# Performance work log

Measured on AMD Instinct MI355X. Metric: run time of the kernel, lower is better.

## Reference

```python
import jax, jax.numpy as jnp
import numpy as np

B, A, V, D = 16, 1024, 1024, 512


def setup_inputs() -> dict:
    key = jax.random.key(0)
    k1, k2 = jax.random.split(key)
    audio_encoded = jax.random.normal(k1, (B, A, D), dtype=jnp.float32)
    visual_encoded = jax.random.normal(k2, (B, V, D), dtype=jnp.float32)
    return {"audio_encoded": audio_encoded, "visual_encoded": visual_encoded}


def reference(audio_encoded, visual_encoded):
    # Batched pairwise L2 distance: out[b, a, v] = ||audio[b,a] - visual[b,v]||_2
    # Fused ||a||^2 + ||v||^2 - 2 a.v formulation (single batched GEMM) replacing
    # the original per-(batch, audio-frame) Python loop of diff/pow/sum/sqrt.
    a_sq = jnp.sum(audio_encoded * audio_encoded, axis=-1)   # [B, A]
    v_sq = jnp.sum(visual_encoded * visual_encoded, axis=-1)  # [B, V]
    cross = jnp.einsum("bad,bvd->bav", audio_encoded, visual_encoded)  # [B, A, V]
    dist_sq = a_sq[:, :, None] + v_sq[:, None, :] - 2.0 * cross
    dist_sq = jnp.maximum(dist_sq, 0.0)  # clamp fp round-off negatives
    l2_features = jnp.sqrt(dist_sq)  # [B, A, V]
    return l2_features
```

## Files before the change

### kernel.cpp

```cpp
#include <hip/hip_runtime.h>
#include <hip/hip_bf16.h>

typedef __attribute__((ext_vector_type(8))) short short8;
typedef __attribute__((ext_vector_type(4))) float fv4;
typedef __attribute__((ext_vector_type(4))) int   iv4;

constexpr int B_ = 16, A_ = 1024, V_ = 1024, D_ = 512;
constexpr int ROWS_A = B_ * A_;
constexpr int ROWS_T = 2 * ROWS_A;
constexpr size_t BF_ONE = (size_t)ROWS_A * D_ * 2;
constexpr size_t WS_NEED = 2 * BF_ONE + (size_t)ROWS_T * 4;

__device__ __forceinline__ unsigned f2bf(float f) {
    unsigned u = __builtin_bit_cast(unsigned, f);
    return (u + 0x7fffu + ((u >> 16) & 1u)) >> 16;
}

__global__ void __launch_bounds__(256)
convert_kernel(const float* __restrict__ audio, const float* __restrict__ visual,
               ushort* __restrict__ abf, ushort* __restrict__ vbf,
               float* __restrict__ normA, float* __restrict__ normV)
{
    const int lane = threadIdx.x & 63;
    const int wv   = (blockIdx.x * 256 + threadIdx.x) >> 6;
    const int nw   = (gridDim.x * 256) >> 6;

    for (int row = wv; row < ROWS_T; row += nw) {
        const float* src; ushort* dst; float* nd; int r;
        if (row < ROWS_A) { src = audio;  dst = abf; nd = normA; r = row; }
        else              { src = visual; dst = vbf; nd = normV; r = row - ROWS_A; }

        const float* p = src + (size_t)r * D_ + lane * 8;
        fv4 x0 = *(const fv4*)p;
        fv4 x1 = *(const fv4*)(p + 4);

        float s = 0.f;
#pragma unroll
        for (int i = 0; i < 4; ++i) s += x0[i] * x0[i] + x1[i] * x1[i];

        iv4 w;
        w[0] = (int)(f2bf(x0[0]) | (f2bf(x0[1]) << 16));
        w[1] = (int)(f2bf(x0[2]) | (f2bf(x0[3]) << 16));
        w[2] = (int)(f2bf(x1[0]) | (f2bf(x1[1]) << 16));
        w[3] = (int)(f2bf(x1[2]) | (f2bf(x1[3]) << 16));
        *(iv4*)(dst + (size_t)r * D_ + lane * 8) = w;

#pragma unroll
        for (int m = 1; m < 64; m <<= 1) s += __shfl_xor(s, m, 64);
        if (lane == 0) nd[r] = s;
    }
}

__device__ __forceinline__ void gload16(const void* g, void* l) {
    __builtin_amdgcn_global_load_lds((const __attribute__((address_space(1))) void*)g,
                                     (__attribute__((address_space(3))) void*)l,
                                     16, 0, 0);
}
__device__ __forceinline__ unsigned lds_addr(const void* p) {
    return (unsigned)(unsigned long long)(__attribute__((address_space(3))) const char*)p;
}
__device__ __forceinline__ short8 dsr128(unsigned a) {
    short8 r;
    asm volatile("ds_read_b128 %0, %1" : "=v"(r) : "v"(a));
    return r;
}
#define SB0()   __builtin_amdgcn_sched_barrier(0)
#define LGK0()  asm volatile("s_waitcnt lgkmcnt(0)")
#define VMCN(n) asm volatile("s_waitcnt vmcnt(" #n ")")
#define RBAR()  do { SB0(); __builtin_amdgcn_s_barrier(); SB0(); } while (0)

__global__ void __launch_bounds__(256, 2)
gemm128(const ushort* __restrict__ abf, const ushort* __restrict__ vbf,
        const float* __restrict__ normA, const float* __restrict__ normV,
        float* __restrict__ out)
{
    __shared__ __align__(16) char sA[2][128 * 128];
    __shared__ __align__(16) char sB[2][128 * 128];
    __shared__ float lnrm[256];

    const int t = threadIdx.x, lane = t & 63, w = t >> 6;
    const int wm = w >> 1, wn = w & 1;

    const int orig = blockIdx.x;
    const int wg   = (orig & 7) * 128 + (orig >> 3);
    const int b = wg >> 6, tile = wg & 63, ab = tile >> 3, vb = tile & 7;

    const ushort* Ag = abf + ((size_t)b * A_ + ab * 128) * D_;
    const ushort* Vg = vbf + ((size_t)b * V_ + vb * 128) * D_;

    const int rl = lane >> 3;
    const int cs = (lane & 7) ^ rl;
    const ushort* asrc = Ag + (size_t)(w * 32 + rl) * D_ + cs * 8;
    const ushort* vsrc = Vg + (size_t)(w * 32 + rl) * D_ + cs * 8;

#define STAGE(kt, buf) do {                                           \
        const size_t _ko = (size_t)(kt) * 64;                         \
        char* _da = (char*)sA[buf] + w * 32 * 128;                    \
        char* _db = (char*)sB[buf] + w * 32 * 128;                    \
        gload16(asrc + 0 * 8 * D_ + _ko, _da + 0 * 1024);             \
        gload16(vsrc + 0 * 8 * D_ + _ko, _db + 0 * 1024);             \
        gload16(asrc + 1 * 8 * D_ + _ko, _da + 1 * 1024);             \
        gload16(vsrc + 1 * 8 * D_ + _ko, _db + 1 * 1024);             \
        gload16(asrc + 2 * 8 * D_ + _ko, _da + 2 * 1024);             \
        gload16(vsrc + 2 * 8 * D_ + _ko, _db + 2 * 1024);             \
        gload16(asrc + 3 * 8 * D_ + _ko, _da + 3 * 1024);             \
        gload16(vsrc + 3 * 8 * D_ + _ko, _db + 3 * 1024);             \
    } while (0)

    if (t < 128) lnrm[t] = normA[(size_t)b * A_ + ab * 128 + t];
    else         lnrm[t] = normV[(size_t)b * V_ + vb * 128 + (t - 128)];
    __syncthreads();

    STAGE(0, 0);
    STAGE(1, 1);
    VMCN(8);
    RBAR();

    fv4 acc[4][4];
#pragma unroll
    for (int m = 0; m < 4; ++m)
#pragma unroll
        for (int n = 0; n < 4; ++n) acc[m][n] = fv4{0.f, 0.f, 0.f, 0.f};

    const int frow = lane & 15, fg = lane >> 4, xk = frow & 7;
    const unsigned cof0 = (unsigned)(((0 + fg) ^ xk) << 4);
    const unsigned cof1 = (unsigned)(((4 + fg) ^ xk) << 4);
    const unsigned baseA = lds_addr(&sA[0][0]);
    const unsigned baseB = lds_addr(&sB[0][0]);
    const unsigned arow = (unsigned)((wm * 64 + frow) * 128);
    const unsigned brow = (unsigned)((wn * 64 + frow) * 128);

#pragma unroll 1
    for (int kt = 0; kt < 8; ++kt) {
        const int cur = kt & 1;
        const unsigned Ab = baseA + (unsigned)cur * 16384u + arow;
        const unsigned Bb = baseB + (unsigned)cur * 16384u + brow;

        short8 av[4][2];
        {
            short8 bv[2][2];
#pragma unroll
            for (int m = 0; m < 4; ++m) {
                av[m][0] = dsr128(Ab + m * 2048 + cof0);
                av[m][1] = dsr128(Ab + m * 2048 + cof1);
            }
#pragma unroll
            for (int n = 0; n < 2; ++n) {
                bv[n][0] = dsr128(Bb + n * 2048 + cof0);
                bv[n][1] = dsr128(Bb + n * 2048 + cof1);
            }
            LGK0(); SB0();
            __builtin_amdgcn_s_setprio(1);
#pragma unroll
            for (int k = 0; k < 2; ++k)
#pragma unroll
                for (int m = 0; m < 4; ++m)
#pragma unroll
                    for (int n = 0; n < 2; ++n)
                        acc[m][n] = __builtin_amdgcn_mfma_f32_16x16x32_bf16(av[m][k], bv[n][k], acc[m][n], 0, 0, 0);
            __builtin_amdgcn_s_setprio(0);
        }
        {
            short8 bv[2][2];
#pragma unroll
            for (int n = 0; n < 2; ++n) {
                bv[n][0] = dsr128(Bb + (n + 2) * 2048 + cof0);
                bv[n][1] = dsr128(Bb + (n + 2) * 2048 + cof1);
            }
            LGK0(); SB0();
            __builtin_amdgcn_s_setprio(1);
#pragma unroll
            for (int k = 0; k < 2; ++k)
#pragma unroll
                for (int m = 0; m < 4; ++m)
#pragma unroll
                    for (int n = 0; n < 2; ++n)
                        acc[m][n + 2] = __builtin_amdgcn_mfma_f32_16x16x32_bf16(av[m][k], bv[n][k], acc[m][n + 2], 0, 0, 0);
            __builtin_amdgcn_s_setprio(0);
        }

        if (kt < 7) {
            RBAR();
            if (kt < 6) {
                STAGE(kt + 2, cur);
                VMCN(8);
            } else {
                VMCN(0);
            }
            RBAR();
        }
    }

    float* Ob = out + (size_t)b * A_ * V_ + (size_t)(ab * 128) * V_ + vb * 128;
#pragma unroll
    for (int m = 0; m < 4; ++m) {
#pragma unroll
        for (int n = 0; n < 4; ++n) {
            const int col = wn * 64 + n * 16 + frow;
            const float vsq = lnrm[128 + col];
#pragma unroll
            for (int j = 0; j < 4; ++j) {
                const int row = wm * 64 + m * 16 + fg * 4 + j;
                float d2 = lnrm[row] + vsq - 2.f * acc[m][n][j];
                Ob[(size_t)row * V_ + col] = sqrtf(fmaxf(d2, 0.f));
            }
        }
    }
#undef STAGE
}

__global__ void __launch_bounds__(256)
l2dist_naive(const float* __restrict__ audio, const float* __restrict__ visual,
             float* __restrict__ out)
{
    const size_t idx = (size_t)blockIdx.x * 256 + threadIdx.x;
    const size_t total = (size_t)B_ * A_ * V_;
    if (idx >= total) return;
    const int v = idx & (V_ - 1);
    const int a = (idx >> 10) & (A_ - 1);
    const int b = idx >> 20;
    const float* ap = audio  + ((size_t)b * A_ + a) * D_;
    const float* vp = visual + ((size_t)b * V_ + v) * D_;
    float s = 0.f;
    for (int d = 0; d < D_; ++d) {
        float df = ap[d] - vp[d];
        s += df * df;
    }
    out[idx] = sqrtf(s);
}

extern "C" void kernel_launch(void* const* d_in, const int* in_sizes, int n_in,
                              void* d_out, int out_size, void* d_ws, size_t ws_size,
                              hipStream_t stream) {
    const float* audio  = (const float*)d_in[0];
    const float* visual = (const float*)d_in[1];
    float* out = (float*)d_out;

    if (ws_size >= WS_NEED) {
        char* ws = (char*)d_ws;
        ushort* abf = (ushort*)ws;
        ushort* vbf = (ushort*)(ws + BF_ONE);
        float*  nA  = (float*)(ws + 2 * BF_ONE);
        float*  nV  = nA + ROWS_A;
        convert_kernel<<<2048, 256, 0, stream>>>(audio, visual, abf, vbf, nA, nV);
        gemm128<<<1024, 256, 0, stream>>>(abf, vbf, nA, nV, out);
    } else {
        const size_t total = (size_t)B_ * A_ * V_;
        l2dist_naive<<<(int)((total + 255) / 256), 256, 0, stream>>>(audio, visual, out);
    }
}
```

Baseline: 49.54 us.

## Enlarge GEMM tile to 256x256 with 512-thread blocks and restructured pipeline

Replaces the 128x128 tile GEMM (256 threads, 2 blocks per CU) with a 256x256 tile using 8 waves, each computing 128x64. LDS doubles to hold larger double-buffered tiles, and the launch drops to 256 blocks, roughly one per CU. The k-loop now waits and synchronises at the top and issues the next stage after the compute, with B and A fragments reloaded in phases. The aim is to cut redundant global and L2 loads through more operand reuse. The cost is no overlap between blocks on a CU, so every CU hits its epilogue store burst at the same time, plus higher register and LDS pressure.

After: 49.49 us. Within noise of the previous version (-0.1%).

```diff
diff --git a/kernel.cpp b/kernel.cpp
--- a/kernel.cpp
+++ b/kernel.cpp
@@ -69,56 +69,54 @@
 #define VMCN(n) asm volatile("s_waitcnt vmcnt(" #n ")")
 #define RBAR()  do { SB0(); __builtin_amdgcn_s_barrier(); SB0(); } while (0)
 
-__global__ void __launch_bounds__(256, 2)
-gemm128(const ushort* __restrict__ abf, const ushort* __restrict__ vbf,
+__global__ void __launch_bounds__(512, 1)
+gemm256(const ushort* __restrict__ abf, const ushort* __restrict__ vbf,
         const float* __restrict__ normA, const float* __restrict__ normV,
         float* __restrict__ out)
 {
-    __shared__ __align__(16) char sA[2][128 * 128];
-    __shared__ __align__(16) char sB[2][128 * 128];
-    __shared__ float lnrm[256];
+    __shared__ __align__(16) char sA[2][256 * 128];
+    __shared__ __align__(16) char sB[2][256 * 128];
+    __shared__ float lnrm[512];
 
     const int t = threadIdx.x, lane = t & 63, w = t >> 6;
-    const int wm = w >> 1, wn = w & 1;
+    const int wm = w >> 2, wn = w & 3;
 
     const int orig = blockIdx.x;
-    const int wg   = (orig & 7) * 128 + (orig >> 3);
-    const int b = wg >> 6, tile = wg & 63, ab = tile >> 3, vb = tile & 7;
-
-    const ushort* Ag = abf + ((size_t)b * A_ + ab * 128) * D_;
-    const ushort* Vg = vbf + ((size_t)b * V_ + vb * 128) * D_;
+    const int wg   = (orig & 7) * 32 + (orig >> 3);
+    const int b = wg >> 4, tile = wg & 15, ab = tile >> 2, vb = tile & 3;
+
+    const ushort* Ag = abf + ((size_t)b * A_ + ab * 256) * D_;
+    const ushort* Vg = vbf + ((size_t)b * V_ + vb * 256) * D_;
 
     const int rl = lane >> 3;
     const int cs = (lane & 7) ^ rl;
-    const ushort* asrc = Ag + (size_t)(w * 32 + rl) * D_ + cs * 8;
-    const ushort* vsrc = Vg + (size_t)(w * 32 + rl) * D_ + cs * 8;
-
-#define STAGE(kt, buf) do {                                           \
-        const size_t _ko = (size_t)(kt) * 64;                         \
-        char* _da = (char*)sA[buf] + w * 32 * 128;                    \
-        char* _db = (char*)sB[buf] + w * 32 * 128;                    \
-        gload16(asrc + 0 * 8 * D_ + _ko, _da + 0 * 1024);             \
-        gload16(vsrc + 0 * 8 * D_ + _ko, _db + 0 * 1024);             \
-        gload16(asrc + 1 * 8 * D_ + _ko, _da + 1 * 1024);             \
-        gload16(vsrc + 1 * 8 * D_ + _ko, _db + 1 * 1024);             \
-        gload16(asrc + 2 * 8 * D_ + _ko, _da + 2 * 1024);             \
-        gload16(vsrc + 2 * 8 * D_ + _ko, _db + 2 * 1024);             \
-        gload16(asrc + 3 * 8 * D_ + _ko, _da + 3 * 1024);             \
-        gload16(vsrc + 3 * 8 * D_ + _ko, _db + 3 * 1024);             \
+    const ushort* asrc = Ag + (size_t)(w * 8 + rl) * D_ + cs * 8;
+    const ushort* vsrc = Vg + (size_t)(w * 8 + rl) * D_ + cs * 8;
+
+#define STAGE(kt, buf) do {                                               \
+        const size_t _ko = (size_t)(kt) * 64;                             \
+        char* _da = (char*)sA[buf] + w * 8 * 128;                         \
+        char* _db = (char*)sB[buf] + w * 8 * 128;                         \
+        gload16(asrc + 0 * 64 * D_ + _ko, _da + 0 * 64 * 128);            \
+        gload16(vsrc + 0 * 64 * D_ + _ko, _db + 0 * 64 * 128);            \
+        gload16(asrc + 1 * 64 * D_ + _ko, _da + 1 * 64 * 128);            \
+        gload16(vsrc + 1 * 64 * D_ + _ko, _db + 1 * 64 * 128);            \
+        gload16(asrc + 2 * 64 * D_ + _ko, _da + 2 * 64 * 128);            \
+        gload16(vsrc + 2 * 64 * D_ + _ko, _db + 2 * 64 * 128);            \
+        gload16(asrc + 3 * 64 * D_ + _ko, _da + 3 * 64 * 128);            \
+        gload16(vsrc + 3 * 64 * D_ + _ko, _db + 3 * 64 * 128);            \
     } while (0)
 
-    if (t < 128) lnrm[t] = normA[(size_t)b * A_ + ab * 128 + t];
-    else         lnrm[t] = normV[(size_t)b * V_ + vb * 128 + (t - 128)];
+    if (t < 256) lnrm[t] = normA[(size_t)b * A_ + ab * 256 + t];
+    else         lnrm[t] = normV[(size_t)b * V_ + vb * 256 + (t - 256)];
     __syncthreads();
 
     STAGE(0, 0);
     STAGE(1, 1);
-    VMCN(8);
-    RBAR();
-
-    fv4 acc[4][4];
-#pragma unroll
-    for (int m = 0; m < 4; ++m)
+
+    fv4 acc[8][4];
+#pragma unroll
+    for (int m = 0; m < 8; ++m)
 #pragma unroll
         for (int n = 0; n < 4; ++n) acc[m][n] = fv4{0.f, 0.f, 0.f, 0.f};
 
@@ -127,80 +125,97 @@
     const unsigned cof1 = (unsigned)(((4 + fg) ^ xk) << 4);
     const unsigned baseA = lds_addr(&sA[0][0]);
     const unsigned baseB = lds_addr(&sB[0][0]);
-    const unsigned arow = (unsigned)((wm * 64 + frow) * 128);
+    const unsigned arow = (unsigned)((wm * 128 + frow) * 128);
     const unsigned brow = (unsigned)((wn * 64 + frow) * 128);
+
+    short8 av[4][2], bv[4][2];
 
 #pragma unroll 1
     for (int kt = 0; kt < 8; ++kt) {
         const int cur = kt & 1;
-        const unsigned Ab = baseA + (unsigned)cur * 16384u + arow;
-        const unsigned Bb = baseB + (unsigned)cur * 16384u + brow;
-
-        short8 av[4][2];
-        {
-            short8 bv[2][2];
-#pragma unroll
-            for (int m = 0; m < 4; ++m) {
-                av[m][0] = dsr128(Ab + m * 2048 + cof0);
-                av[m][1] = dsr128(Ab + m * 2048 + cof1);
-            }
-#pragma unroll
-            for (int n = 0; n < 2; ++n) {
-                bv[n][0] = dsr128(Bb + n * 2048 + cof0);
-                bv[n][1] = dsr128(Bb + n * 2048 + cof1);
-            }
-            LGK0(); SB0();
-            __builtin_amdgcn_s_setprio(1);
-#pragma unroll
-            for (int k = 0; k < 2; ++k)
-#pragma unroll
-                for (int m = 0; m < 4; ++m)
-#pragma unroll
-                    for (int n = 0; n < 2; ++n)
-                        acc[m][n] = __builtin_amdgcn_mfma_f32_16x16x32_bf16(av[m][k], bv[n][k], acc[m][n], 0, 0, 0);
-            __builtin_amdgcn_s_setprio(0);
-        }
-        {
-            short8 bv[2][2];
-#pragma unroll
-            for (int n = 0; n < 2; ++n) {
-                bv[n][0] = dsr128(Bb + (n + 2) * 2048 + cof0);
-                bv[n][1] = dsr128(Bb + (n + 2) * 2048 + cof1);
-            }
-            LGK0(); SB0();
-            __builtin_amdgcn_s_setprio(1);
-#pragma unroll
-            for (int k = 0; k < 2; ++k)
-#pragma unroll
-                for (int m = 0; m < 4; ++m)
-#pragma unroll
-                    for (int n = 0; n < 2; ++n)
-                        acc[m][n + 2] = __builtin_amdgcn_mfma_f32_16x16x32_bf16(av[m][k], bv[n][k], acc[m][n + 2], 0, 0, 0);
-            __builtin_amdgcn_s_setprio(0);
-        }
-
-        if (kt < 7) {
-            RBAR();
-            if (kt < 6) {
-                STAGE(kt + 2, cur);
-                VMCN(8);
-            } else {
-                VMCN(0);
-            }
-            RBAR();
-        }
-    }
-
-    float* Ob = out + (size_t)b * A_ * V_ + (size_t)(ab * 128) * V_ + vb * 128;
-#pragma unroll
-    for (int m = 0; m < 4; ++m) {
+        const unsigned Ab = baseA + (unsigned)cur * 32768u + arow;
+        const unsigned Bb = baseB + (unsigned)cur * 32768u + brow;
+
+        if (kt < 7) { VMCN(8); } else { VMCN(0); }
+        RBAR();
+
+#pragma unroll
+        for (int m = 0; m < 4; ++m) {
+            av[m][0] = dsr128(Ab + m * 2048 + cof0);
+            av[m][1] = dsr128(Ab + m * 2048 + cof1);
+        }
+#pragma unroll
+        for (int n = 0; n < 2; ++n) {
+            bv[n][0] = dsr128(Bb + n * 2048 + cof0);
+            bv[n][1] = dsr128(Bb + n * 2048 + cof1);
+        }
+        LGK0(); SB0();
+        __builtin_amdgcn_s_setprio(1);
+#pragma unroll
+        for (int k = 0; k < 2; ++k)
+#pragma unroll
+            for (int m = 0; m < 4; ++m)
+#pragma unroll
+                for (int n = 0; n < 2; ++n)
+                    acc[m][n] = __builtin_amdgcn_mfma_f32_16x16x32_bf16(av[m][k], bv[n][k], acc[m][n], 0, 0, 0);
+        __builtin_amdgcn_s_setprio(0);
+
+#pragma unroll
+        for (int n = 2; n < 4; ++n) {
+            bv[n][0] = dsr128(Bb + n * 2048 + cof0);
+            bv[n][1] = dsr128(Bb + n * 2048 + cof1);
+        }
+        LGK0(); SB0();
+        __builtin_amdgcn_s_setprio(1);
+#pragma unroll
+        for (int k = 0; k < 2; ++k)
+#pragma unroll
+            for (int m = 0; m < 4; ++m)
+#pragma unroll
+                for (int n = 2; n < 4; ++n)
+                    acc[m][n] = __builtin_amdgcn_mfma_f32_16x16x32_bf16(av[m][k], bv[n][k], acc[m][n], 0, 0, 0);
+        __builtin_amdgcn_s_setprio(0);
+
+#pragma unroll
+        for (int m = 0; m < 4; ++m) {
+            av[m][0] = dsr128(Ab + (m + 4) * 2048 + cof0);
+            av[m][1] = dsr128(Ab + (m + 4) * 2048 + cof1);
+        }
+        LGK0(); SB0();
+        __builtin_amdgcn_s_setprio(1);
+#pragma unroll
+        for (int k = 0; k < 2; ++k)
+#pragma unroll
+            for (int m = 0; m < 4; ++m)
+#pragma unroll
+                for (int n = 2; n < 4; ++n)
+                    acc[m + 4][n] = __builtin_amdgcn_mfma_f32_16x16x32_bf16(av[m][k], bv[n][k], acc[m + 4][n], 0, 0, 0);
+        __builtin_amdgcn_s_setprio(0);
+
+        __builtin_amdgcn_s_setprio(1);
+#pragma unroll
+        for (int k = 0; k < 2; ++k)
+#pragma unroll
+            for (int m = 0; m < 4; ++m)
+#pragma unroll
+                for (int n = 0; n < 2; ++n)
+                    acc[m + 4][n] = __builtin_amdgcn_mfma_f32_16x16x32_bf16(av[m][k], bv[n][k], acc[m + 4][n], 0, 0, 0);
+        __builtin_amdgcn_s_setprio(0);
+
+        RBAR();
+        if (kt < 6) STAGE(kt + 2, cur);
+    }
+
+    float* Ob = out + (size_t)b * A_ * V_ + (size_t)(ab * 256) * V_ + vb * 256;
+#pragma unroll
+    for (int m = 0; m < 8; ++m) {
 #pragma unroll
         for (int n = 0; n < 4; ++n) {
             const int col = wn * 64 + n * 16 + frow;
-            const float vsq = lnrm[128 + col];
+            const float vsq = lnrm[256 + col];
 #pragma unroll
             for (int j = 0; j < 4; ++j) {
-                const int row = wm * 64 + m * 16 + fg * 4 + j;
+                const int row = wm * 128 + m * 16 + fg * 4 + j;
                 float d2 = lnrm[row] + vsq - 2.f * acc[m][n][j];
                 Ob[(size_t)row * V_ + col] = sqrtf(fmaxf(d2, 0.f));
             }
@@ -243,7 +258,7 @@
         float*  nA  = (float*)(ws + 2 * BF_ONE);
         float*  nV  = nA + ROWS_A;
         convert_kernel<<<2048, 256, 0, stream>>>(audio, visual, abf, vbf, nA, nV);
-        gemm128<<<1024, 256, 0, stream>>>(abf, vbf, nA, nV, out);
+        gemm256<<<256, 512, 0, stream>>>(abf, vbf, nA, nV, out);
     } else {
         const size_t total = (size_t)B_ * A_ * V_;
         l2dist_naive<<<(int)((total + 255) / 256), 256, 0, stream>>>(audio, visual, out);
```

## Drop LDS double buffering for single buffer and higher occupancy

Applied to the files above, without the earlier changes.

Replaces the two-stage LDS ping-pong with a single 32 KB buffer and raises the launch bound from 2 to 4 blocks per CU. Each k-step now syncs, issues the global-to-LDS loads for the next tile, and syncs again, leaving the compiler to insert the vmcnt wait. The aim is to hide memory latency through more resident workgroups instead of in-block prefetch. In exchange, loads no longer overlap with MFMA work inside a block, and the tighter register budget from the higher launch bound may cause spills.

Result: slower. 60.69 us (+22.5%).

```diff
diff --git a/kernel.cpp b/kernel.cpp
--- a/kernel.cpp
+++ b/kernel.cpp
@@ -64,18 +64,16 @@
     asm volatile("ds_read_b128 %0, %1" : "=v"(r) : "v"(a));
     return r;
 }
-#define SB0()   __builtin_amdgcn_sched_barrier(0)
-#define LGK0()  asm volatile("s_waitcnt lgkmcnt(0)")
-#define VMCN(n) asm volatile("s_waitcnt vmcnt(" #n ")")
-#define RBAR()  do { SB0(); __builtin_amdgcn_s_barrier(); SB0(); } while (0)
-
-__global__ void __launch_bounds__(256, 2)
+#define SB0()  __builtin_amdgcn_sched_barrier(0)
+#define LGK0() asm volatile("s_waitcnt lgkmcnt(0)")
+
+__global__ void __launch_bounds__(256, 4)
 gemm128(const ushort* __restrict__ abf, const ushort* __restrict__ vbf,
         const float* __restrict__ normA, const float* __restrict__ normV,
         float* __restrict__ out)
 {
-    __shared__ __align__(16) char sA[2][128 * 128];
-    __shared__ __align__(16) char sB[2][128 * 128];
+    __shared__ __align__(16) char sA[128 * 128];
+    __shared__ __align__(16) char sB[128 * 128];
     __shared__ float lnrm[256];
 
     const int t = threadIdx.x, lane = t & 63, w = t >> 6;
@@ -93,10 +91,10 @@
     const ushort* asrc = Ag + (size_t)(w * 32 + rl) * D_ + cs * 8;
     const ushort* vsrc = Vg + (size_t)(w * 32 + rl) * D_ + cs * 8;
 
-#define STAGE(kt, buf) do {                                           \
+#define STAGE(kt) do {                                                \
         const size_t _ko = (size_t)(kt) * 64;                         \
-        char* _da = (char*)sA[buf] + w * 32 * 128;                    \
-        char* _db = (char*)sB[buf] + w * 32 * 128;                    \
+        char* _da = (char*)sA + w * 32 * 128;                         \
+        char* _db = (char*)sB + w * 32 * 128;                         \
         gload16(asrc + 0 * 8 * D_ + _ko, _da + 0 * 1024);             \
         gload16(vsrc + 0 * 8 * D_ + _ko, _db + 0 * 1024);             \
         gload16(asrc + 1 * 8 * D_ + _ko, _da + 1 * 1024);             \
@@ -109,12 +107,9 @@
 
     if (t < 128) lnrm[t] = normA[(size_t)b * A_ + ab * 128 + t];
     else         lnrm[t] = normV[(size_t)b * V_ + vb * 128 + (t - 128)];
+
+    STAGE(0);
     __syncthreads();
-
-    STAGE(0, 0);
-    STAGE(1, 1);
-    VMCN(8);
-    RBAR();
 
     fv4 acc[4][4];
 #pragma unroll
@@ -125,17 +120,11 @@
     const int frow = lane & 15, fg = lane >> 4, xk = frow & 7;
     const unsigned cof0 = (unsigned)(((0 + fg) ^ xk) << 4);
     const unsigned cof1 = (unsigned)(((4 + fg) ^ xk) << 4);
-    const unsigned baseA = lds_addr(&sA[0][0]);
-    const unsigned baseB = lds_addr(&sB[0][0]);
-    const unsigned arow = (unsigned)((wm * 64 + frow) * 128);
-    const unsigned brow = (unsigned)((wn * 64 + frow) * 128);
+    const unsigned Ab = lds_addr(&sA[0]) + (unsigned)((wm * 64 + frow) * 128);
+    const unsigned Bb = lds_addr(&sB[0]) + (unsigned)((wn * 64 + frow) * 128);
 
 #pragma unroll 1
     for (int kt = 0; kt < 8; ++kt) {
-        const int cur = kt & 1;
-        const unsigned Ab = baseA + (unsigned)cur * 16384u + arow;
-        const unsigned Bb = baseB + (unsigned)cur * 16384u + brow;
-
         short8 av[4][2];
         {
             short8 bv[2][2];
@@ -180,14 +169,9 @@
         }
 
         if (kt < 7) {
-            RBAR();
-            if (kt < 6) {
-                STAGE(kt + 2, cur);
-                VMCN(8);
-            } else {
-                VMCN(0);
-            }
-            RBAR();
+            __syncthreads();
+            STAGE(kt + 1);
+            __syncthreads();
         }
     }
 
```
